# Optimization experiments

Hardware: AMD Instinct MI355X
Metric: run time of the kernel (lower is better)

The kernel has to match this reference:

```python
import jax, jax.numpy as jnp
import numpy as np

B = 64      # graphs per batch
N = 1024    # nodes per graph (equal-size graphs -> static top-k)
D = 256     # in_dim
DEG = 16    # avg degree
K = 512     # k = ratio * N, ratio = 0.5
E = B * N * DEG
NT = B * N


def setup_inputs() -> dict:
    key = jax.random.key(0)
    ks = jax.random.split(key, 8)
    feature = jax.random.normal(ks[0], (NT, D), jnp.float32)
    gid = jnp.repeat(jnp.arange(B), N * DEG)          # graph id per edge
    src = gid * N + jax.random.randint(ks[1], (E,), 0, N)
    dst = gid * N + jax.random.randint(ks[2], (E,), 0, N)
    label = jax.random.randint(ks[3], (B,), 0, 2)
    W = jax.random.normal(ks[4], (D, 1), jnp.float32) / np.sqrt(D)   # GraphConv weight
    b = jnp.zeros((1,), jnp.float32)                                  # GraphConv bias
    lin1_w = jax.random.normal(ks[5], (2, 1), jnp.float32) / np.sqrt(2.0)
    lin1_b = jnp.zeros((1,), jnp.float32)
    return dict(feature=feature, src=src, dst=dst, label=label,
                W=W, b=b, lin1_w=lin1_w, lin1_b=lin1_b)


def reference(feature, src, dst, label, W, b, lin1_w, lin1_b):
    fdt = feature.dtype
    # ---- get_bias_score: distance-to-class-center score ----
    node_label = jnp.repeat(label, N).astype(fdt)                 # [NT]
    gemb = feature.reshape(B, N, D).mean(axis=1)                  # AvgPooling per graph [B, D]
    lab_f = label.astype(fdt)                                     # [B]
    n1 = jnp.maximum(lab_f.sum(), 1.0)
    n0 = jnp.maximum((1.0 - lab_f).sum(), 1.0)
    center0 = (gemb * (1.0 - lab_f)[:, None]).sum(0) / n0         # [D]
    center1 = (gemb * lab_f[:, None]).sum(0) / n1                 # [D]
    d0 = jnp.sqrt(((feature - center0) ** 2).sum(-1))             # [NT]
    d1 = jnp.sqrt(((feature - center1) ** 2).sum(-1))             # [NT]
    score_distance = (d0 - d1) * ((node_label - 0.5) * 2.0)       # [NT]
    # ---- GraphConv(in_dim, 1), norm='both' (DGL semantics) ----
    ones_e = jnp.ones((E,), fdt)
    deg_out = jax.ops.segment_sum(ones_e, src, NT)
    deg_in = jax.ops.segment_sum(ones_e, dst, NT)
    ns = jnp.maximum(deg_out, 1.0) ** -0.5                        # src-side norm
    nd = jnp.maximum(deg_in, 1.0) ** -0.5                         # dst-side norm
    h = (feature @ W) * ns[:, None]                               # project first (out<in) [NT,1]
    agg = jax.ops.segment_sum(h[src], dst, NT)                    # [NT,1]
    score_gcn = (agg * nd[:, None] + b)[:, 0]                     # [NT]
    # ---- combine two scores with lin1: Linear(2, 1) ----
    score = jnp.stack([score_gcn, score_distance], axis=-1) @ lin1_w + lin1_b  # [NT,1]
    sflat = score[:, 0]
    # ---- per-graph top-k (mytopk with equal-size graphs -> static k) ----
    _, idx = jax.lax.top_k(sflat.reshape(B, N), K)                # [B,K] local indices
    perm = (idx + (jnp.arange(B) * N)[:, None]).reshape(-1)       # [B*K] global indices
    mask = jnp.ones((NT,), bool).at[perm].set(False)
    perm_com = jnp.nonzero(mask, size=NT - B * K)[0]              # complement, static size
    # ---- gather + tanh-gated features ----
    feature_dis = feature[perm] * jnp.tanh(sflat[perm])[:, None]          # [B*K, D]
    feature_com = feature[perm_com] * jnp.tanh(sflat[perm_com])[:, None]  # [B*(N-K), D]
    score_soft = jax.nn.softmax(score, axis=0)                    # softmax over all nodes
    return feature_dis, feature_com, perm, perm_com, score_soft
```

## Files before the change

kernel.cpp:

```cpp
#include <hip/hip_runtime.h>
#include <math.h>

#define Bg   64
#define Nn   1024
#define Dd   256
#define Ee   (Bg * Nn * 16)
#define EPG  16384
#define NT   (Bg * Nn)
#define Kk   512

#define OFF_DIS   0
#define OFF_COM   8388608
#define OFF_PERM  16777216
#define OFF_PCOM  16809984
#define OFF_SOFT  16842752

#define WS_SGCN    0
#define WS_H0      (NT * 4)
#define WS_SFLAT   (NT * 4 * 2)
#define WS_GPART   (NT * 4 * 3)
#define WS_C0      (WS_GPART + 512 * 256 * 4)
#define WS_C1      (WS_C0 + 1024)
#define WS_REDM    (WS_C1 + 1024)
#define WS_REDS    (WS_REDM + 256)
#define WS_PERMI   (WS_REDS + 256)
#define WS_PCOMI   (WS_PERMI + 32768 * 4)

__global__ void k_pass1(const float* __restrict__ f, const float* __restrict__ W,
                        float* __restrict__ gpart, float* __restrict__ h0) {
    __shared__ float scol[4 * Dd];
    int blk  = blockIdx.x;
    int base = blk * 128;
    int t    = threadIdx.x;
    int lane = t & 63, wid = t >> 6;
    const float4* f4 = (const float4*)f;
    const float4* W4 = (const float4*)W;
    float4 w = W4[lane];
    float4 cs = make_float4(0.f, 0.f, 0.f, 0.f);
    for (int r = 0; r < 32; ++r) {
        int row = base + wid * 32 + r;
        float4 v = f4[(size_t)row * 64 + lane];
        cs.x += v.x; cs.y += v.y; cs.z += v.z; cs.w += v.w;
        float d = v.x * w.x + v.y * w.y + v.z * w.z + v.w * w.w;
        for (int o = 32; o > 0; o >>= 1) d += __shfl_xor(d, o);
        if (lane == 0) h0[row] = d;
    }
    ((float4*)scol)[wid * 64 + lane] = cs;
    __syncthreads();
    float s = scol[t] + scol[Dd + t] + scol[2 * Dd + t] + scol[3 * Dd + t];
    gpart[blk * Dd + t] = s;
}

__global__ __launch_bounds__(1024) void k_edges(
        const int* __restrict__ src, const int* __restrict__ dst,
        const float* __restrict__ h0, const float* __restrict__ b,
        const float* __restrict__ gpart, const int* __restrict__ label,
        float* __restrict__ sgcn, float* __restrict__ c0, float* __restrict__ c1) {
    __shared__ ushort2 eb[EPG];
    __shared__ int   sdo[Nn];
    __shared__ int   sdi[Nn];
    __shared__ float sagg[Nn];
    __shared__ float shn[Nn];
    int g = blockIdx.x, t = threadIdx.x;
    sdo[t] = 0; sdi[t] = 0; sagg[t] = 0.f;
    __syncthreads();
    int ebase = g * EPG;
    const int4* s4 = (const int4*)(src + ebase);
    const int4* d4 = (const int4*)(dst + ebase);
    #pragma unroll
    for (int i = t; i < EPG / 4; i += 1024) {
        int4 ss = s4[i];
        int4 dd = d4[i];
        int s0 = ss.x & (Nn - 1), s1 = ss.y & (Nn - 1), s2 = ss.z & (Nn - 1), s3 = ss.w & (Nn - 1);
        int e0 = dd.x & (Nn - 1), e1 = dd.y & (Nn - 1), e2 = dd.z & (Nn - 1), e3 = dd.w & (Nn - 1);
        eb[i * 4 + 0] = make_ushort2((unsigned short)s0, (unsigned short)e0);
        eb[i * 4 + 1] = make_ushort2((unsigned short)s1, (unsigned short)e1);
        eb[i * 4 + 2] = make_ushort2((unsigned short)s2, (unsigned short)e2);
        eb[i * 4 + 3] = make_ushort2((unsigned short)s3, (unsigned short)e3);
        atomicAdd(&sdo[s0], 1); atomicAdd(&sdo[s1], 1);
        atomicAdd(&sdo[s2], 1); atomicAdd(&sdo[s3], 1);
        atomicAdd(&sdi[e0], 1); atomicAdd(&sdi[e1], 1);
        atomicAdd(&sdi[e2], 1); atomicAdd(&sdi[e3], 1);
    }
    __syncthreads();
    {
        int dg = sdo[t]; if (dg < 1) dg = 1;
        shn[t] = h0[g * Nn + t] / sqrtf((float)dg);
    }
    __syncthreads();
    #pragma unroll
    for (int i = t; i < EPG; i += 1024) {
        ushort2 e = eb[i];
        atomicAdd(&sagg[e.y], shn[e.x]);
    }
    __syncthreads();
    {
        int dg = sdi[t]; if (dg < 1) dg = 1;
        float nd = 1.f / sqrtf((float)dg);
        sgcn[g * Nn + t] = sagg[t] * nd + b[0];
    }
    if (g == 0 && t < Dd) {
        int n1 = 0;
        for (int gg = 0; gg < Bg; ++gg) n1 += label[gg];
        float fn1 = fmaxf((float)n1, 1.f);
        float fn0 = fmaxf((float)(Bg - n1), 1.f);
        float s0 = 0.f, s1 = 0.f;
        for (int gg = 0; gg < Bg; ++gg) {
            float v = 0.f;
            for (int p = 0; p < 8; ++p) v += gpart[(gg * 8 + p) * Dd + t];
            v *= (1.f / (float)Nn);
            if (label[gg]) s1 += v; else s0 += v;
        }
        c0[t] = s0 / fn0;
        c1[t] = s1 / fn1;
    }
}

__global__ void k_score(const float* __restrict__ f, const float* __restrict__ c0,
                        const float* __restrict__ c1, const float* __restrict__ sgcn,
                        const int* __restrict__ label, const float* __restrict__ lw,
                        const float* __restrict__ lb, float* __restrict__ sflat) {
    int node = blockIdx.x * 4 + (threadIdx.x >> 6);
    int lane = threadIdx.x & 63;
    const float4* f4  = (const float4*)f;
    const float4* c04 = (const float4*)c0;
    const float4* c14 = (const float4*)c1;
    float4 v = f4[(size_t)node * 64 + lane];
    float4 a = c04[lane];
    float4 bb = c14[lane];
    float dx, acc0, acc1;
    dx = v.x - a.x;  acc0  = dx * dx;
    dx = v.y - a.y;  acc0 += dx * dx;
    dx = v.z - a.z;  acc0 += dx * dx;
    dx = v.w - a.w;  acc0 += dx * dx;
    dx = v.x - bb.x; acc1  = dx * dx;
    dx = v.y - bb.y; acc1 += dx * dx;
    dx = v.z - bb.z; acc1 += dx * dx;
    dx = v.w - bb.w; acc1 += dx * dx;
    for (int o = 32; o > 0; o >>= 1) {
        acc0 += __shfl_xor(acc0, o);
        acc1 += __shfl_xor(acc1, o);
    }
    if (lane == 0) {
        float d0 = sqrtf(acc0), d1 = sqrtf(acc1);
        int g = node >> 10;
        float sgn = label[g] ? 1.f : -1.f;
        float sdist = (d0 - d1) * sgn;
        sflat[node] = sgcn[node] * lw[0] + sdist * lw[1] + lb[0];
    }
}

__global__ __launch_bounds__(512) void k_topk(
        const float* __restrict__ sflat, int* __restrict__ permI,
        int* __restrict__ pcomI, float* __restrict__ out,
        float* __restrict__ redM, float* __restrict__ redS) {
    __shared__ unsigned long long sk[1024];
    __shared__ int   sflag[1024];
    __shared__ int   swave[8];
    __shared__ float sred[16];
    int g = blockIdx.x, t = threadIdx.x;
    int lane = t & 63, w = t >> 6;
    float v0 = sflat[g * Nn + t];
    float v1 = sflat[g * Nn + t + 512];
    unsigned u0 = __float_as_uint(v0);
    unsigned u1 = __float_as_uint(v1);
    unsigned o0 = u0 ^ ((u0 >> 31) ? 0xFFFFFFFFu : 0x80000000u);
    unsigned o1 = u1 ^ ((u1 >> 31) ? 0xFFFFFFFFu : 0x80000000u);
    sk[t]       = ((unsigned long long)o0 << 32) | (unsigned)(1023 - t);
    sk[t + 512] = ((unsigned long long)o1 << 32) | (unsigned)(1023 - (t + 512));
    __syncthreads();
    for (int k = 2; k <= 1024; k <<= 1) {
        for (int j = k >> 1; j > 0; j >>= 1) {
            int l = ((t & ~(j - 1)) << 1) | (t & (j - 1));
            int r = l | j;
            unsigned long long a = sk[l], bk = sk[r];
            bool up = ((l & k) == 0);
            if ((a < bk) == up) { sk[l] = bk; sk[r] = a; }
            __syncthreads();
        }
    }
    sflag[t] = 1; sflag[t + 512] = 1;
    __syncthreads();
    {
        int loc = 1023 - (int)(sk[t] & 0xFFFFFFFFu);
        sflag[loc] = 0;
        int gi = g * Nn + loc;
        permI[g * Kk + t] = gi;
        out[OFF_PERM + g * Kk + t] = (float)gi;
    }
    __syncthreads();
    int f0 = sflag[2 * t], f1 = sflag[2 * t + 1];
    int f2 = f0 + f1;
    int inc = f2;
    for (int o = 1; o < 64; o <<= 1) {
        int y = __shfl_up(inc, o);
        if (lane >= o) inc += y;
    }
    if (lane == 63) swave[w] = inc;
    __syncthreads();
    if (t < 8) {
        int a = swave[t];
        for (int o = 1; o < 8; o <<= 1) {
            int y = __shfl_up(a, o);
            if (t >= o) a += y;
        }
        swave[t] = a;
    }
    __syncthreads();
    int basep = ((w > 0) ? swave[w - 1] : 0) + (inc - f2);
    if (f0) {
        int gi = g * Nn + 2 * t;
        pcomI[g * Kk + basep] = gi;
        out[OFF_PCOM + g * Kk + basep] = (float)gi;
    }
    if (f1) {
        int pos = basep + f0;
        int gi = g * Nn + 2 * t + 1;
        pcomI[g * Kk + pos] = gi;
        out[OFF_PCOM + g * Kk + pos] = (float)gi;
    }
    float m = fmaxf(v0, v1);
    for (int o = 32; o > 0; o >>= 1) m = fmaxf(m, __shfl_xor(m, o));
    if (lane == 0) sred[w] = m;
    __syncthreads();
    if (t < 8) {
        float a = sred[t];
        for (int o = 4; o > 0; o >>= 1) a = fmaxf(a, __shfl_xor(a, o));
        if (t == 0) sred[0] = a;
    }
    __syncthreads();
    m = sred[0];
    float s = expf(v0 - m) + expf(v1 - m);
    for (int o = 32; o > 0; o >>= 1) s += __shfl_xor(s, o);
    if (lane == 0) sred[8 + w] = s;
    __syncthreads();
    if (t < 8) {
        float a = sred[8 + t];
        for (int o = 4; o > 0; o >>= 1) a += __shfl_xor(a, o);
        if (t == 0) { redM[g] = m; redS[g] = a; }
    }
}

__global__ void k_write(const float* __restrict__ f, const int* __restrict__ permI,
                        const int* __restrict__ pcomI, const float* __restrict__ sflat,
                        const float* __restrict__ redM, const float* __restrict__ redS,
                        float* __restrict__ out) {
    __shared__ float sMS[2];
    int t = threadIdx.x;
    if (t < 64) {
        float m = redM[t];
        float mm = m;
        for (int o = 32; o > 0; o >>= 1) mm = fmaxf(mm, __shfl_xor(mm, o));
        float s = redS[t] * expf(m - mm);
        for (int o = 32; o > 0; o >>= 1) s += __shfl_xor(s, o);
        if (t == 0) { sMS[0] = mm; sMS[1] = s; }
    }
    __syncthreads();
    float M = sMS[0], S = sMS[1];
    if (t < 4) {
        int i = blockIdx.x * 4 + t;
        out[OFF_SOFT + i] = expf(sflat[i] - M) / S;
    }
    int j = blockIdx.x * 4 + (t >> 6);
    int lane = t & 63;
    int row = (j < 32768) ? permI[j] : pcomI[j - 32768];
    float tv = tanhf(sflat[row]);
    const float4* f4 = (const float4*)f;
    float4* o4 = (float4*)out;
    float4 v = f4[(size_t)row * 64 + lane];
    o4[(size_t)j * 64 + lane] = make_float4(v.x * tv, v.y * tv, v.z * tv, v.w * tv);
}

extern "C" void kernel_launch(void* const* d_in, const int* in_sizes, int n_in,
                              void* d_out, int out_size, void* d_ws, size_t ws_size,
                              hipStream_t stream) {
    const float* feature = (const float*)d_in[0];
    const int*   src     = (const int*)d_in[1];
    const int*   dst     = (const int*)d_in[2];
    const int*   label   = (const int*)d_in[3];
    const float* W       = (const float*)d_in[4];
    const float* b       = (const float*)d_in[5];
    const float* lw      = (const float*)d_in[6];
    const float* lb      = (const float*)d_in[7];
    float* out = (float*)d_out;
    char*  ws  = (char*)d_ws;

    float* sgcn    = (float*)(ws + WS_SGCN);
    float* h0      = (float*)(ws + WS_H0);
    float* sflat   = (float*)(ws + WS_SFLAT);
    float* gpart   = (float*)(ws + WS_GPART);
    float* c0      = (float*)(ws + WS_C0);
    float* c1      = (float*)(ws + WS_C1);
    float* redM    = (float*)(ws + WS_REDM);
    float* redS    = (float*)(ws + WS_REDS);
    int*   permI   = (int*)(ws + WS_PERMI);
    int*   pcomI   = (int*)(ws + WS_PCOMI);

    k_pass1<<<512, 256, 0, stream>>>(feature, W, gpart, h0);
    k_edges<<<Bg, 1024, 0, stream>>>(src, dst, h0, b, gpart, label, sgcn, c0, c1);
    k_score<<<NT / 4, 256, 0, stream>>>(feature, c0, c1, sgcn, label, lw, lb, sflat);
    k_topk<<<Bg, 512, 0, stream>>>(sflat, permI, pcomI, out, redM, redS);
    k_write<<<NT / 4, 256, 0, stream>>>(feature, permI, pcomI, sflat, redM, redS, out);
}
```

Before: 223.9 us.

## Split edge processing into 4 slices per graph and overlap with feature pass

```diff
diff --git a/kernel.cpp b/kernel.cpp
--- a/kernel.cpp
+++ b/kernel.cpp
@@ -6,6 +6,7 @@
 #define Dd   256
 #define Ee   (Bg * Nn * 16)
 #define EPG  16384
+#define EPB  4096
 #define NT   (Bg * Nn)
 #define Kk   512
 
@@ -15,91 +16,115 @@
 #define OFF_PCOM  16809984
 #define OFF_SOFT  16842752
 
-#define WS_SGCN    0
-#define WS_H0      (NT * 4)
-#define WS_SFLAT   (NT * 4 * 2)
-#define WS_GPART   (NT * 4 * 3)
+#define WS_H0      0
+#define WS_SFLAT   (NT * 4)
+#define WS_GPART   (NT * 4 * 2)
 #define WS_C0      (WS_GPART + 512 * 256 * 4)
 #define WS_C1      (WS_C0 + 1024)
 #define WS_REDM    (WS_C1 + 1024)
 #define WS_REDS    (WS_REDM + 256)
 #define WS_PERMI   (WS_REDS + 256)
 #define WS_PCOMI   (WS_PERMI + 32768 * 4)
-
-__global__ void k_pass1(const float* __restrict__ f, const float* __restrict__ W,
-                        float* __restrict__ gpart, float* __restrict__ h0) {
-    __shared__ float scol[4 * Dd];
-    int blk  = blockIdx.x;
-    int base = blk * 128;
-    int t    = threadIdx.x;
-    int lane = t & 63, wid = t >> 6;
-    const float4* f4 = (const float4*)f;
-    const float4* W4 = (const float4*)W;
-    float4 w = W4[lane];
-    float4 cs = make_float4(0.f, 0.f, 0.f, 0.f);
-    for (int r = 0; r < 32; ++r) {
-        int row = base + wid * 32 + r;
-        float4 v = f4[(size_t)row * 64 + lane];
-        cs.x += v.x; cs.y += v.y; cs.z += v.z; cs.w += v.w;
-        float d = v.x * w.x + v.y * w.y + v.z * w.z + v.w * w.w;
-        for (int o = 32; o > 0; o >>= 1) d += __shfl_xor(d, o);
-        if (lane == 0) h0[row] = d;
-    }
-    ((float4*)scol)[wid * 64 + lane] = cs;
-    __syncthreads();
-    float s = scol[t] + scol[Dd + t] + scol[2 * Dd + t] + scol[3 * Dd + t];
-    gpart[blk * Dd + t] = s;
-}
-
-__global__ __launch_bounds__(1024) void k_edges(
+#define WS_EPACK   (WS_PCOMI + 32768 * 4)
+#define WS_DO4     (WS_EPACK + Ee * 4)
+#define WS_DI4     (WS_DO4 + 4 * NT * 4)
+#define WS_AGG4    (WS_DI4 + 4 * NT * 4)
+
+__global__ __launch_bounds__(256) void k_mix(
+        const float* __restrict__ f, const float* __restrict__ W,
         const int* __restrict__ src, const int* __restrict__ dst,
-        const float* __restrict__ h0, const float* __restrict__ b,
-        const float* __restrict__ gpart, const int* __restrict__ label,
-        float* __restrict__ sgcn, float* __restrict__ c0, float* __restrict__ c1) {
-    __shared__ ushort2 eb[EPG];
-    __shared__ int   sdo[Nn];
-    __shared__ int   sdi[Nn];
+        float* __restrict__ gpart, float* __restrict__ h0,
+        unsigned* __restrict__ epack, int* __restrict__ do4, int* __restrict__ di4) {
+    __shared__ int smem[2048];
+    int blk = blockIdx.x;
+    int t   = threadIdx.x;
+    if (blk < 512) {
+        float* scol = (float*)smem;
+        int base = blk * 128;
+        int lane = t & 63, wid = t >> 6;
+        const float4* f4 = (const float4*)f;
+        const float4* W4 = (const float4*)W;
+        float4 w = W4[lane];
+        float4 cs = make_float4(0.f, 0.f, 0.f, 0.f);
+        for (int r = 0; r < 32; ++r) {
+            int row = base + wid * 32 + r;
+            float4 v = f4[(size_t)row * 64 + lane];
+            cs.x += v.x; cs.y += v.y; cs.z += v.z; cs.w += v.w;
+            float d = v.x * w.x + v.y * w.y + v.z * w.z + v.w * w.w;
+            for (int o = 32; o > 0; o >>= 1) d += __shfl_xor(d, o);
+            if (lane == 0) h0[row] = d;
+        }
+        ((float4*)scol)[wid * 64 + lane] = cs;
+        __syncthreads();
+        float s = scol[t] + scol[Dd + t] + scol[2 * Dd + t] + scol[3 * Dd + t];
+        gpart[blk * Dd + t] = s;
+    } else {
+        int* sdo = smem;
+        int* sdi = smem + 1024;
+        int blk2 = blk - 512;
+        int g = blk2 >> 2, sl = blk2 & 3;
+        #pragma unroll
+        for (int j = 0; j < 4; ++j) { sdo[t + j * 256] = 0; sdi[t + j * 256] = 0; }
+        __syncthreads();
+        int ebase = g * EPG + sl * EPB;
+        const int4* s4 = (const int4*)(src + ebase);
+        const int4* d4 = (const int4*)(dst + ebase);
+        uint4* p4 = (uint4*)(epack + ebase);
+        #pragma unroll
+        for (int i = t; i < EPB / 4; i += 256) {
+            int4 ss = s4[i];
+            int4 dd = d4[i];
+            int s0 = ss.x & (Nn - 1), s1 = ss.y & (Nn - 1), s2 = ss.z & (Nn - 1), s3 = ss.w & (Nn - 1);
+            int e0 = dd.x & (Nn - 1), e1 = dd.y & (Nn - 1), e2 = dd.z & (Nn - 1), e3 = dd.w & (Nn - 1);
+            uint4 pk;
+            pk.x = (unsigned)(s0 | (e0 << 16));
+            pk.y = (unsigned)(s1 | (e1 << 16));
+            pk.z = (unsigned)(s2 | (e2 << 16));
+            pk.w = (unsigned)(s3 | (e3 << 16));
+            p4[i] = pk;
+            atomicAdd(&sdo[s0], 1); atomicAdd(&sdo[s1], 1);
+            atomicAdd(&sdo[s2], 1); atomicAdd(&sdo[s3], 1);
+            atomicAdd(&sdi[e0], 1); atomicAdd(&sdi[e1], 1);
+            atomicAdd(&sdi[e2], 1); atomicAdd(&sdi[e3], 1);
+        }
+        __syncthreads();
+        int base = sl * NT + g * Nn;
+        #pragma unroll
+        for (int j = 0; j < 4; ++j) {
+            do4[base + t + j * 256] = sdo[t + j * 256];
+            di4[base + t + j * 256] = sdi[t + j * 256];
+        }
+    }
+}
+
+__global__ __launch_bounds__(1024) void k_edgeB(
+        const unsigned* __restrict__ epack, const float* __restrict__ h0,
+        const int* __restrict__ do4, const float* __restrict__ gpart,
+        const int* __restrict__ label, float* __restrict__ agg4,
+        float* __restrict__ c0, float* __restrict__ c1) {
+    __shared__ float shn[Nn];
     __shared__ float sagg[Nn];
-    __shared__ float shn[Nn];
-    int g = blockIdx.x, t = threadIdx.x;
-    sdo[t] = 0; sdi[t] = 0; sagg[t] = 0.f;
-    __syncthreads();
-    int ebase = g * EPG;
-    const int4* s4 = (const int4*)(src + ebase);
-    const int4* d4 = (const int4*)(dst + ebase);
-    #pragma unroll
-    for (int i = t; i < EPG / 4; i += 1024) {
-        int4 ss = s4[i];
-        int4 dd = d4[i];
-        int s0 = ss.x & (Nn - 1), s1 = ss.y & (Nn - 1), s2 = ss.z & (Nn - 1), s3 = ss.w & (Nn - 1);
-        int e0 = dd.x & (Nn - 1), e1 = dd.y & (Nn - 1), e2 = dd.z & (Nn - 1), e3 = dd.w & (Nn - 1);
-        eb[i * 4 + 0] = make_ushort2((unsigned short)s0, (unsigned short)e0);
-        eb[i * 4 + 1] = make_ushort2((unsigned short)s1, (unsigned short)e1);
-        eb[i * 4 + 2] = make_ushort2((unsigned short)s2, (unsigned short)e2);
-        eb[i * 4 + 3] = make_ushort2((unsigned short)s3, (unsigned short)e3);
-        atomicAdd(&sdo[s0], 1); atomicAdd(&sdo[s1], 1);
-        atomicAdd(&sdo[s2], 1); atomicAdd(&sdo[s3], 1);
-        atomicAdd(&sdi[e0], 1); atomicAdd(&sdi[e1], 1);
-        atomicAdd(&sdi[e2], 1); atomicAdd(&sdi[e3], 1);
-    }
-    __syncthreads();
+    int blk = blockIdx.x, t = threadIdx.x;
+    int g = blk >> 2, sl = blk & 3;
     {
-        int dg = sdo[t]; if (dg < 1) dg = 1;
-        shn[t] = h0[g * Nn + t] / sqrtf((float)dg);
-    }
-    __syncthreads();
-    #pragma unroll
-    for (int i = t; i < EPG; i += 1024) {
-        ushort2 e = eb[i];
-        atomicAdd(&sagg[e.y], shn[e.x]);
+        int idx = g * Nn + t;
+        int dg = do4[idx] + do4[NT + idx] + do4[2 * NT + idx] + do4[3 * NT + idx];
+        if (dg < 1) dg = 1;
+        shn[t] = h0[idx] / sqrtf((float)dg);
+        sagg[t] = 0.f;
     }
     __syncthreads();
     {
-        int dg = sdi[t]; if (dg < 1) dg = 1;
-        float nd = 1.f / sqrtf((float)dg);
-        sgcn[g * Nn + t] = sagg[t] * nd + b[0];
-    }
-    if (g == 0 && t < Dd) {
+        const uint4* p4 = (const uint4*)(epack + g * EPG + sl * EPB);
+        uint4 pk = p4[t];
+        atomicAdd(&sagg[pk.x >> 16], shn[pk.x & 0xFFFF]);
+        atomicAdd(&sagg[pk.y >> 16], shn[pk.y & 0xFFFF]);
+        atomicAdd(&sagg[pk.z >> 16], shn[pk.z & 0xFFFF]);
+        atomicAdd(&sagg[pk.w >> 16], shn[pk.w & 0xFFFF]);
+    }
+    __syncthreads();
+    agg4[sl * NT + g * Nn + t] = sagg[t];
+    if (blk == 0 && t < Dd) {
         int n1 = 0;
         for (int gg = 0; gg < Bg; ++gg) n1 += label[gg];
         float fn1 = fmaxf((float)n1, 1.f);
@@ -117,8 +142,9 @@
 }
 
 __global__ void k_score(const float* __restrict__ f, const float* __restrict__ c0,
-                        const float* __restrict__ c1, const float* __restrict__ sgcn,
-                        const int* __restrict__ label, const float* __restrict__ lw,
+                        const float* __restrict__ c1, const float* __restrict__ agg4,
+                        const int* __restrict__ di4, const int* __restrict__ label,
+                        const float* __restrict__ b, const float* __restrict__ lw,
                         const float* __restrict__ lb, float* __restrict__ sflat) {
     int node = blockIdx.x * 4 + (threadIdx.x >> 6);
     int lane = threadIdx.x & 63;
@@ -146,7 +172,11 @@
         int g = node >> 10;
         float sgn = label[g] ? 1.f : -1.f;
         float sdist = (d0 - d1) * sgn;
-        sflat[node] = sgcn[node] * lw[0] + sdist * lw[1] + lb[0];
+        float agg = agg4[node] + agg4[NT + node] + agg4[2 * NT + node] + agg4[3 * NT + node];
+        int dg = di4[node] + di4[NT + node] + di4[2 * NT + node] + di4[3 * NT + node];
+        if (dg < 1) dg = 1;
+        float sgcn = agg / sqrtf((float)dg) + b[0];
+        sflat[node] = sgcn * lw[0] + sdist * lw[1] + lb[0];
     }
 }
 
@@ -285,20 +315,23 @@
     float* out = (float*)d_out;
     char*  ws  = (char*)d_ws;
 
-    float* sgcn    = (float*)(ws + WS_SGCN);
-    float* h0      = (float*)(ws + WS_H0);
-    float* sflat   = (float*)(ws + WS_SFLAT);
-    float* gpart   = (float*)(ws + WS_GPART);
-    float* c0      = (float*)(ws + WS_C0);
-    float* c1      = (float*)(ws + WS_C1);
-    float* redM    = (float*)(ws + WS_REDM);
-    float* redS    = (float*)(ws + WS_REDS);
-    int*   permI   = (int*)(ws + WS_PERMI);
-    int*   pcomI   = (int*)(ws + WS_PCOMI);
-
-    k_pass1<<<512, 256, 0, stream>>>(feature, W, gpart, h0);
-    k_edges<<<Bg, 1024, 0, stream>>>(src, dst, h0, b, gpart, label, sgcn, c0, c1);
-    k_score<<<NT / 4, 256, 0, stream>>>(feature, c0, c1, sgcn, label, lw, lb, sflat);
+    float*    h0    = (float*)(ws + WS_H0);
+    float*    sflat = (float*)(ws + WS_SFLAT);
+    float*    gpart = (float*)(ws + WS_GPART);
+    float*    c0    = (float*)(ws + WS_C0);
+    float*    c1    = (float*)(ws + WS_C1);
+    float*    redM  = (float*)(ws + WS_REDM);
+    float*    redS  = (float*)(ws + WS_REDS);
+    int*      permI = (int*)(ws + WS_PERMI);
+    int*      pcomI = (int*)(ws + WS_PCOMI);
+    unsigned* epack = (unsigned*)(ws + WS_EPACK);
+    int*      do4   = (int*)(ws + WS_DO4);
+    int*      di4   = (int*)(ws + WS_DI4);
+    float*    agg4  = (float*)(ws + WS_AGG4);
+
+    k_mix<<<768, 256, 0, stream>>>(feature, W, src, dst, gpart, h0, epack, do4, di4);
+    k_edgeB<<<256, 1024, 0, stream>>>(epack, h0, do4, gpart, label, agg4, c0, c1);
+    k_score<<<NT / 4, 256, 0, stream>>>(feature, c0, c1, agg4, di4, label, b, lw, lb, sflat);
     k_topk<<<Bg, 512, 0, stream>>>(sflat, permI, pcomI, out, redM, redS);
     k_write<<<NT / 4, 256, 0, stream>>>(feature, permI, pcomI, sflat, redM, redS, out);
 }
```

After: 211.0 us. 1.06x faster.

## Fuse all stages into one persistent kernel with software grid barriers

Applied to the files above, without the earlier changes.

```diff
diff --git a/kernel.cpp b/kernel.cpp
--- a/kernel.cpp
+++ b/kernel.cpp
@@ -4,271 +4,300 @@
 #define Bg   64
 #define Nn   1024
 #define Dd   256
-#define Ee   (Bg * Nn * 16)
 #define EPG  16384
-#define NT   (Bg * Nn)
+#define EPB  4096
+#define NT   65536
 #define Kk   512
 
-#define OFF_DIS   0
-#define OFF_COM   8388608
 #define OFF_PERM  16777216
 #define OFF_PCOM  16809984
 #define OFF_SOFT  16842752
 
-#define WS_SGCN    0
-#define WS_H0      (NT * 4)
-#define WS_SFLAT   (NT * 4 * 2)
-#define WS_GPART   (NT * 4 * 3)
-#define WS_C0      (WS_GPART + 512 * 256 * 4)
-#define WS_C1      (WS_C0 + 1024)
-#define WS_REDM    (WS_C1 + 1024)
-#define WS_REDS    (WS_REDM + 256)
-#define WS_PERMI   (WS_REDS + 256)
-#define WS_PCOMI   (WS_PERMI + 32768 * 4)
-
-__global__ void k_pass1(const float* __restrict__ f, const float* __restrict__ W,
-                        float* __restrict__ gpart, float* __restrict__ h0) {
-    __shared__ float scol[4 * Dd];
-    int blk  = blockIdx.x;
-    int base = blk * 128;
-    int t    = threadIdx.x;
-    int lane = t & 63, wid = t >> 6;
-    const float4* f4 = (const float4*)f;
-    const float4* W4 = (const float4*)W;
-    float4 w = W4[lane];
-    float4 cs = make_float4(0.f, 0.f, 0.f, 0.f);
-    for (int r = 0; r < 32; ++r) {
-        int row = base + wid * 32 + r;
-        float4 v = f4[(size_t)row * 64 + lane];
-        cs.x += v.x; cs.y += v.y; cs.z += v.z; cs.w += v.w;
-        float d = v.x * w.x + v.y * w.y + v.z * w.z + v.w * w.w;
-        for (int o = 32; o > 0; o >>= 1) d += __shfl_xor(d, o);
-        if (lane == 0) h0[row] = d;
-    }
-    ((float4*)scol)[wid * 64 + lane] = cs;
-    __syncthreads();
-    float s = scol[t] + scol[Dd + t] + scol[2 * Dd + t] + scol[3 * Dd + t];
-    gpart[blk * Dd + t] = s;
+#define WS_BAR    0
+#define WS_H0     256
+#define WS_SFLAT  (WS_H0 + NT * 4)
+#define WS_GPART  (WS_SFLAT + NT * 4)
+#define WS_DO4    (WS_GPART + 256 * 256 * 4)
+#define WS_DI4    (WS_DO4 + 4 * NT * 4)
+#define WS_AGG4   (WS_DI4 + 4 * NT * 4)
+#define WS_REDM   (WS_AGG4 + 4 * NT * 4)
+#define WS_REDS   (WS_REDM + 256 * 4)
+#define WS_PERMI  (WS_REDS + 256 * 4)
+#define WS_PCOMI  (WS_PERMI + 32768 * 4)
+
+__device__ __forceinline__ void gridbar(int* ctr, int target) {
+    __syncthreads();
+    if (threadIdx.x == 0) {
+        __threadfence();
+        __hip_atomic_fetch_add(ctr, 1, __ATOMIC_RELEASE, __HIP_MEMORY_SCOPE_AGENT);
+        while (__hip_atomic_load(ctr, __ATOMIC_ACQUIRE, __HIP_MEMORY_SCOPE_AGENT) < target)
+            __builtin_amdgcn_s_sleep(8);
+        __threadfence();
+    }
+    __syncthreads();
 }
 
-__global__ __launch_bounds__(1024) void k_edges(
+__global__ __launch_bounds__(1024, 4) void k_all(
+        const float* __restrict__ f, const float* __restrict__ W,
         const int* __restrict__ src, const int* __restrict__ dst,
-        const float* __restrict__ h0, const float* __restrict__ b,
-        const float* __restrict__ gpart, const int* __restrict__ label,
-        float* __restrict__ sgcn, float* __restrict__ c0, float* __restrict__ c1) {
-    __shared__ ushort2 eb[EPG];
+        const int* __restrict__ label, const float* __restrict__ bias,
+        const float* __restrict__ lw, const float* __restrict__ lb,
+        float* __restrict__ out, int* __restrict__ bar,
+        float* __restrict__ h0, float* __restrict__ sflat,
+        float* __restrict__ gpart, int* __restrict__ do4, int* __restrict__ di4,
+        float* __restrict__ agg4, float* __restrict__ redM, float* __restrict__ redS,
+        int* __restrict__ permI, int* __restrict__ pcomI) {
+    __shared__ unsigned epk[EPB];
+    __shared__ float scol[4096];
     __shared__ int   sdo[Nn];
     __shared__ int   sdi[Nn];
+    __shared__ float shn[Nn];
     __shared__ float sagg[Nn];
-    __shared__ float shn[Nn];
-    int g = blockIdx.x, t = threadIdx.x;
-    sdo[t] = 0; sdi[t] = 0; sagg[t] = 0.f;
-    __syncthreads();
-    int ebase = g * EPG;
-    const int4* s4 = (const int4*)(src + ebase);
-    const int4* d4 = (const int4*)(dst + ebase);
-    #pragma unroll
-    for (int i = t; i < EPG / 4; i += 1024) {
-        int4 ss = s4[i];
-        int4 dd = d4[i];
-        int s0 = ss.x & (Nn - 1), s1 = ss.y & (Nn - 1), s2 = ss.z & (Nn - 1), s3 = ss.w & (Nn - 1);
-        int e0 = dd.x & (Nn - 1), e1 = dd.y & (Nn - 1), e2 = dd.z & (Nn - 1), e3 = dd.w & (Nn - 1);
-        eb[i * 4 + 0] = make_ushort2((unsigned short)s0, (unsigned short)e0);
-        eb[i * 4 + 1] = make_ushort2((unsigned short)s1, (unsigned short)e1);
-        eb[i * 4 + 2] = make_ushort2((unsigned short)s2, (unsigned short)e2);
-        eb[i * 4 + 3] = make_ushort2((unsigned short)s3, (unsigned short)e3);
+    __shared__ float cpart[2048];
+    __shared__ float c0s[Dd], c1s[Dd];
+    __shared__ unsigned long long sk[1024];
+    __shared__ int   sflag[1024];
+    __shared__ int   swave[8];
+    __shared__ float sred[16];
+
+    int b = blockIdx.x, t = threadIdx.x;
+    int lane = t & 63, w = t >> 6;
+    int g = b >> 2, sl = b & 3;
+    const float4* f4 = (const float4*)f;
+
+    sdo[t] = 0; sdi[t] = 0;
+    int4 ss = ((const int4*)(src + g * EPG + sl * EPB))[t];
+    int4 dd = ((const int4*)(dst + g * EPG + sl * EPB))[t];
+    __syncthreads();
+    {
+        float4 wv = ((const float4*)W)[lane];
+        float4 cs = make_float4(0.f, 0.f, 0.f, 0.f);
+        int rbase = b * 256 + w * 16;
+        for (int r = 0; r < 16; ++r) {
+            float4 v = f4[(size_t)(rbase + r) * 64 + lane];
+            cs.x += v.x; cs.y += v.y; cs.z += v.z; cs.w += v.w;
+            float d = v.x * wv.x + v.y * wv.y + v.z * wv.z + v.w * wv.w;
+            for (int o = 32; o > 0; o >>= 1) d += __shfl_xor(d, o);
+            if (lane == 0) h0[rbase + r] = d;
+        }
+        ((float4*)scol)[w * 64 + lane] = cs;
+    }
+    {
+        int s0 = ss.x & 1023, s1 = ss.y & 1023, s2 = ss.z & 1023, s3 = ss.w & 1023;
+        int e0 = dd.x & 1023, e1 = dd.y & 1023, e2 = dd.z & 1023, e3 = dd.w & 1023;
+        uint4 pk;
+        pk.x = (unsigned)(s0 | (e0 << 16));
+        pk.y = (unsigned)(s1 | (e1 << 16));
+        pk.z = (unsigned)(s2 | (e2 << 16));
+        pk.w = (unsigned)(s3 | (e3 << 16));
+        ((uint4*)epk)[t] = pk;
         atomicAdd(&sdo[s0], 1); atomicAdd(&sdo[s1], 1);
         atomicAdd(&sdo[s2], 1); atomicAdd(&sdo[s3], 1);
         atomicAdd(&sdi[e0], 1); atomicAdd(&sdi[e1], 1);
         atomicAdd(&sdi[e2], 1); atomicAdd(&sdi[e3], 1);
     }
     __syncthreads();
-    {
-        int dg = sdo[t]; if (dg < 1) dg = 1;
-        shn[t] = h0[g * Nn + t] / sqrtf((float)dg);
-    }
-    __syncthreads();
-    #pragma unroll
-    for (int i = t; i < EPG; i += 1024) {
-        ushort2 e = eb[i];
-        atomicAdd(&sagg[e.y], shn[e.x]);
-    }
-    __syncthreads();
-    {
-        int dg = sdi[t]; if (dg < 1) dg = 1;
-        float nd = 1.f / sqrtf((float)dg);
-        sgcn[g * Nn + t] = sagg[t] * nd + b[0];
-    }
-    if (g == 0 && t < Dd) {
+    if (t < 256) {
+        float s = 0.f;
+        for (int q = 0; q < 16; ++q) s += scol[q * 256 + t];
+        gpart[b * 256 + t] = s;
+    }
+    do4[sl * NT + g * Nn + t] = sdo[t];
+    di4[sl * NT + g * Nn + t] = sdi[t];
+    gridbar(bar, 256);
+
+    {
+        int q = t >> 8, c = t & 255;
         int n1 = 0;
         for (int gg = 0; gg < Bg; ++gg) n1 += label[gg];
-        float fn1 = fmaxf((float)n1, 1.f);
-        float fn0 = fmaxf((float)(Bg - n1), 1.f);
         float s0 = 0.f, s1 = 0.f;
-        for (int gg = 0; gg < Bg; ++gg) {
-            float v = 0.f;
-            for (int p = 0; p < 8; ++p) v += gpart[(gg * 8 + p) * Dd + t];
-            v *= (1.f / (float)Nn);
-            if (label[gg]) s1 += v; else s0 += v;
-        }
-        c0[t] = s0 / fn0;
-        c1[t] = s1 / fn1;
-    }
-}
-
-__global__ void k_score(const float* __restrict__ f, const float* __restrict__ c0,
-                        const float* __restrict__ c1, const float* __restrict__ sgcn,
-                        const int* __restrict__ label, const float* __restrict__ lw,
-                        const float* __restrict__ lb, float* __restrict__ sflat) {
-    int node = blockIdx.x * 4 + (threadIdx.x >> 6);
-    int lane = threadIdx.x & 63;
-    const float4* f4  = (const float4*)f;
-    const float4* c04 = (const float4*)c0;
-    const float4* c14 = (const float4*)c1;
-    float4 v = f4[(size_t)node * 64 + lane];
-    float4 a = c04[lane];
-    float4 bb = c14[lane];
-    float dx, acc0, acc1;
-    dx = v.x - a.x;  acc0  = dx * dx;
-    dx = v.y - a.y;  acc0 += dx * dx;
-    dx = v.z - a.z;  acc0 += dx * dx;
-    dx = v.w - a.w;  acc0 += dx * dx;
-    dx = v.x - bb.x; acc1  = dx * dx;
-    dx = v.y - bb.y; acc1 += dx * dx;
-    dx = v.z - bb.z; acc1 += dx * dx;
-    dx = v.w - bb.w; acc1 += dx * dx;
-    for (int o = 32; o > 0; o >>= 1) {
-        acc0 += __shfl_xor(acc0, o);
-        acc1 += __shfl_xor(acc1, o);
-    }
-    if (lane == 0) {
-        float d0 = sqrtf(acc0), d1 = sqrtf(acc1);
-        int g = node >> 10;
+        for (int bb2 = q * 64; bb2 < q * 64 + 64; ++bb2) {
+            float v = gpart[bb2 * 256 + c];
+            if (label[bb2 >> 2]) s1 += v; else s0 += v;
+        }
+        cpart[q * 256 + c] = s0;
+        cpart[1024 + q * 256 + c] = s1;
+        __syncthreads();
+        if (t < 256) {
+            float a0 = cpart[t] + cpart[256 + t] + cpart[512 + t] + cpart[768 + t];
+            float a1 = cpart[1024 + t] + cpart[1280 + t] + cpart[1536 + t] + cpart[1792 + t];
+            float fn1 = fmaxf((float)n1, 1.f);
+            float fn0 = fmaxf((float)(Bg - n1), 1.f);
+            c0s[t] = (a0 / (float)Nn) / fn0;
+            c1s[t] = (a1 / (float)Nn) / fn1;
+        }
+    }
+    {
+        int node = g * Nn + t;
+        int dg = do4[node] + do4[NT + node] + do4[2 * NT + node] + do4[3 * NT + node];
+        if (dg < 1) dg = 1;
+        shn[t] = h0[node] / sqrtf((float)dg);
+        sagg[t] = 0.f;
+    }
+    __syncthreads();
+    {
+        uint4 pk = ((const uint4*)epk)[t];
+        atomicAdd(&sagg[pk.x >> 16], shn[pk.x & 0xFFFF]);
+        atomicAdd(&sagg[pk.y >> 16], shn[pk.y & 0xFFFF]);
+        atomicAdd(&sagg[pk.z >> 16], shn[pk.z & 0xFFFF]);
+        atomicAdd(&sagg[pk.w >> 16], shn[pk.w & 0xFFFF]);
+    }
+    __syncthreads();
+    agg4[sl * NT + g * Nn + t] = sagg[t];
+    gridbar(bar, 512);
+
+    {
+        float4 a = ((const float4*)c0s)[lane];
+        float4 bb4 = ((const float4*)c1s)[lane];
         float sgn = label[g] ? 1.f : -1.f;
-        float sdist = (d0 - d1) * sgn;
-        sflat[node] = sgcn[node] * lw[0] + sdist * lw[1] + lb[0];
-    }
-}
-
-__global__ __launch_bounds__(512) void k_topk(
-        const float* __restrict__ sflat, int* __restrict__ permI,
-        int* __restrict__ pcomI, float* __restrict__ out,
-        float* __restrict__ redM, float* __restrict__ redS) {
-    __shared__ unsigned long long sk[1024];
-    __shared__ int   sflag[1024];
-    __shared__ int   swave[8];
-    __shared__ float sred[16];
-    int g = blockIdx.x, t = threadIdx.x;
-    int lane = t & 63, w = t >> 6;
-    float v0 = sflat[g * Nn + t];
-    float v1 = sflat[g * Nn + t + 512];
-    unsigned u0 = __float_as_uint(v0);
-    unsigned u1 = __float_as_uint(v1);
-    unsigned o0 = u0 ^ ((u0 >> 31) ? 0xFFFFFFFFu : 0x80000000u);
-    unsigned o1 = u1 ^ ((u1 >> 31) ? 0xFFFFFFFFu : 0x80000000u);
-    sk[t]       = ((unsigned long long)o0 << 32) | (unsigned)(1023 - t);
-    sk[t + 512] = ((unsigned long long)o1 << 32) | (unsigned)(1023 - (t + 512));
-    __syncthreads();
-    for (int k = 2; k <= 1024; k <<= 1) {
-        for (int j = k >> 1; j > 0; j >>= 1) {
-            int l = ((t & ~(j - 1)) << 1) | (t & (j - 1));
-            int r = l | j;
-            unsigned long long a = sk[l], bk = sk[r];
-            bool up = ((l & k) == 0);
-            if ((a < bk) == up) { sk[l] = bk; sk[r] = a; }
-            __syncthreads();
-        }
-    }
-    sflag[t] = 1; sflag[t + 512] = 1;
-    __syncthreads();
-    {
-        int loc = 1023 - (int)(sk[t] & 0xFFFFFFFFu);
-        sflag[loc] = 0;
-        int gi = g * Nn + loc;
-        permI[g * Kk + t] = gi;
-        out[OFF_PERM + g * Kk + t] = (float)gi;
-    }
-    __syncthreads();
-    int f0 = sflag[2 * t], f1 = sflag[2 * t + 1];
-    int f2 = f0 + f1;
-    int inc = f2;
-    for (int o = 1; o < 64; o <<= 1) {
-        int y = __shfl_up(inc, o);
-        if (lane >= o) inc += y;
-    }
-    if (lane == 63) swave[w] = inc;
-    __syncthreads();
-    if (t < 8) {
-        int a = swave[t];
-        for (int o = 1; o < 8; o <<= 1) {
-            int y = __shfl_up(a, o);
-            if (t >= o) a += y;
-        }
-        swave[t] = a;
-    }
-    __syncthreads();
-    int basep = ((w > 0) ? swave[w - 1] : 0) + (inc - f2);
-    if (f0) {
-        int gi = g * Nn + 2 * t;
-        pcomI[g * Kk + basep] = gi;
-        out[OFF_PCOM + g * Kk + basep] = (float)gi;
-    }
-    if (f1) {
-        int pos = basep + f0;
-        int gi = g * Nn + 2 * t + 1;
-        pcomI[g * Kk + pos] = gi;
-        out[OFF_PCOM + g * Kk + pos] = (float)gi;
-    }
-    float m = fmaxf(v0, v1);
-    for (int o = 32; o > 0; o >>= 1) m = fmaxf(m, __shfl_xor(m, o));
-    if (lane == 0) sred[w] = m;
-    __syncthreads();
-    if (t < 8) {
-        float a = sred[t];
-        for (int o = 4; o > 0; o >>= 1) a = fmaxf(a, __shfl_xor(a, o));
-        if (t == 0) sred[0] = a;
-    }
-    __syncthreads();
-    m = sred[0];
-    float s = expf(v0 - m) + expf(v1 - m);
-    for (int o = 32; o > 0; o >>= 1) s += __shfl_xor(s, o);
-    if (lane == 0) sred[8 + w] = s;
-    __syncthreads();
-    if (t < 8) {
-        float a = sred[8 + t];
-        for (int o = 4; o > 0; o >>= 1) a += __shfl_xor(a, o);
-        if (t == 0) { redM[g] = m; redS[g] = a; }
-    }
-}
-
-__global__ void k_write(const float* __restrict__ f, const int* __restrict__ permI,
-                        const int* __restrict__ pcomI, const float* __restrict__ sflat,
-                        const float* __restrict__ redM, const float* __restrict__ redS,
-                        float* __restrict__ out) {
-    __shared__ float sMS[2];
-    int t = threadIdx.x;
-    if (t < 64) {
-        float m = redM[t];
-        float mm = m;
-        for (int o = 32; o > 0; o >>= 1) mm = fmaxf(mm, __shfl_xor(mm, o));
-        float s = redS[t] * expf(m - mm);
-        for (int o = 32; o > 0; o >>= 1) s += __shfl_xor(s, o);
-        if (t == 0) { sMS[0] = mm; sMS[1] = s; }
-    }
-    __syncthreads();
-    float M = sMS[0], S = sMS[1];
-    if (t < 4) {
-        int i = blockIdx.x * 4 + t;
-        out[OFF_SOFT + i] = expf(sflat[i] - M) / S;
-    }
-    int j = blockIdx.x * 4 + (t >> 6);
-    int lane = t & 63;
-    int row = (j < 32768) ? permI[j] : pcomI[j - 32768];
-    float tv = tanhf(sflat[row]);
-    const float4* f4 = (const float4*)f;
-    float4* o4 = (float4*)out;
-    float4 v = f4[(size_t)row * 64 + lane];
-    o4[(size_t)j * 64 + lane] = make_float4(v.x * tv, v.y * tv, v.z * tv, v.w * tv);
+        float blw0 = lw[0], blw1 = lw[1], blb = lb[0], bbias = bias[0];
+        int rbase = b * 256 + w * 16;
+        for (int r = 0; r < 16; ++r) {
+            int node = rbase + r;
+            float4 v = f4[(size_t)node * 64 + lane];
+            float dx, acc0, acc1;
+            dx = v.x - a.x;   acc0  = dx * dx;
+            dx = v.y - a.y;   acc0 += dx * dx;
+            dx = v.z - a.z;   acc0 += dx * dx;
+            dx = v.w - a.w;   acc0 += dx * dx;
+            dx = v.x - bb4.x; acc1  = dx * dx;
+            dx = v.y - bb4.y; acc1 += dx * dx;
+            dx = v.z - bb4.z; acc1 += dx * dx;
+            dx = v.w - bb4.w; acc1 += dx * dx;
+            for (int o = 32; o > 0; o >>= 1) {
+                acc0 += __shfl_xor(acc0, o);
+                acc1 += __shfl_xor(acc1, o);
+            }
+            if (lane == 0) {
+                float sdist = (sqrtf(acc0) - sqrtf(acc1)) * sgn;
+                float agg = agg4[node] + agg4[NT + node] + agg4[2 * NT + node] + agg4[3 * NT + node];
+                int dg = di4[node] + di4[NT + node] + di4[2 * NT + node] + di4[3 * NT + node];
+                if (dg < 1) dg = 1;
+                float sg = agg / sqrtf((float)dg) + bbias;
+                float sc = sg * blw0 + sdist * blw1 + blb;
+                sflat[node] = sc;
+                scol[w * 16 + r] = sc;
+            }
+        }
+        __syncthreads();
+        if (t < 256) {
+            float m = scol[t];
+            for (int o = 32; o > 0; o >>= 1) m = fmaxf(m, __shfl_xor(m, o));
+            if (lane == 0) sred[t >> 6] = m;
+        }
+        __syncthreads();
+        if (t == 0) sred[8] = fmaxf(fmaxf(sred[0], sred[1]), fmaxf(sred[2], sred[3]));
+        __syncthreads();
+        float M = sred[8];
+        if (t < 256) {
+            float e = expf(scol[t] - M);
+            for (int o = 32; o > 0; o >>= 1) e += __shfl_xor(e, o);
+            if (lane == 0) sred[4 + (t >> 6)] = e;
+        }
+        __syncthreads();
+        if (t == 0) { redM[b] = M; redS[b] = sred[4] + sred[5] + sred[6] + sred[7]; }
+    }
+    gridbar(bar, 768);
+
+    if (b < Bg) {
+        int gg = b;
+        float v = sflat[gg * Nn + t];
+        unsigned u = __float_as_uint(v);
+        unsigned od = u ^ ((u >> 31) ? 0xFFFFFFFFu : 0x80000000u);
+        sk[t] = ((unsigned long long)od << 32) | (unsigned)(1023 - t);
+        __syncthreads();
+        for (int k = 2; k <= 1024; k <<= 1) {
+            for (int j = k >> 1; j > 0; j >>= 1) {
+                if (t < 512) {
+                    int l = ((t & ~(j - 1)) << 1) | (t & (j - 1));
+                    int r = l | j;
+                    unsigned long long a = sk[l], bk = sk[r];
+                    bool up = ((l & k) == 0);
+                    if ((a < bk) == up) { sk[l] = bk; sk[r] = a; }
+                }
+                __syncthreads();
+            }
+        }
+        sflag[t] = 1;
+        __syncthreads();
+        if (t < 512) {
+            int loc = 1023 - (int)(sk[t] & 0xFFFFFFFFu);
+            sflag[loc] = 0;
+            int gi = gg * Nn + loc;
+            permI[gg * Kk + t] = gi;
+            out[OFF_PERM + gg * Kk + t] = (float)gi;
+        }
+        __syncthreads();
+        int f0 = 0, f1 = 0, inc = 0, fsum = 0;
+        if (t < 512) {
+            f0 = sflag[2 * t]; f1 = sflag[2 * t + 1];
+            fsum = f0 + f1;
+            inc = fsum;
+            for (int o = 1; o < 64; o <<= 1) {
+                int y = __shfl_up(inc, o);
+                if (lane >= o) inc += y;
+            }
+            if (lane == 63) swave[w] = inc;
+        }
+        __syncthreads();
+        if (t < 8) {
+            int a = swave[t];
+            for (int o = 1; o < 8; o <<= 1) {
+                int y = __shfl_up(a, o);
+                if (t >= o) a += y;
+            }
+            swave[t] = a;
+        }
+        __syncthreads();
+        if (t < 512) {
+            int basep = ((w > 0) ? swave[w - 1] : 0) + (inc - fsum);
+            if (f0) {
+                int gi = gg * Nn + 2 * t;
+                pcomI[gg * Kk + basep] = gi;
+                out[OFF_PCOM + gg * Kk + basep] = (float)gi;
+            }
+            if (f1) {
+                int pos = basep + f0;
+                int gi = gg * Nn + 2 * t + 1;
+                pcomI[gg * Kk + pos] = gi;
+                out[OFF_PCOM + gg * Kk + pos] = (float)gi;
+            }
+        }
+    }
+    gridbar(bar, 1024);
+
+    {
+        if (t < 256) {
+            float m = redM[t];
+            for (int o = 32; o > 0; o >>= 1) m = fmaxf(m, __shfl_xor(m, o));
+            if (lane == 0) sred[t >> 6] = m;
+        }
+        __syncthreads();
+        if (t == 0) sred[8] = fmaxf(fmaxf(sred[0], sred[1]), fmaxf(sred[2], sred[3]));
+        __syncthreads();
+        float M = sred[8];
+        if (t < 256) {
+            float s = redS[t] * expf(redM[t] - M);
+            for (int o = 32; o > 0; o >>= 1) s += __shfl_xor(s, o);
+            if (lane == 0) sred[4 + (t >> 6)] = s;
+        }
+        __syncthreads();
+        if (t == 0) sred[9] = sred[4] + sred[5] + sred[6] + sred[7];
+        __syncthreads();
+        float S = sred[9];
+        if (t < 256) {
+            int node = b * 256 + t;
+            out[OFF_SOFT + node] = expf(sflat[node] - M) / S;
+        }
+        for (int r = 0; r < 16; ++r) {
+            int j = b * 256 + w * 16 + r;
+            int row = (j < 32768) ? permI[j] : pcomI[j - 32768];
+            float tv = tanhf(sflat[row]);
+            float4 v = f4[(size_t)row * 64 + lane];
+            ((float4*)out)[(size_t)j * 64 + lane] =
+                make_float4(v.x * tv, v.y * tv, v.z * tv, v.w * tv);
+        }
+    }
 }
 
 extern "C" void kernel_launch(void* const* d_in, const int* in_sizes, int n_in,
@@ -279,26 +308,26 @@
     const int*   dst     = (const int*)d_in[2];
     const int*   label   = (const int*)d_in[3];
     const float* W       = (const float*)d_in[4];
-    const float* b       = (const float*)d_in[5];
+    const float* bias    = (const float*)d_in[5];
     const float* lw      = (const float*)d_in[6];
     const float* lb      = (const float*)d_in[7];
     float* out = (float*)d_out;
     char*  ws  = (char*)d_ws;
 
-    float* sgcn    = (float*)(ws + WS_SGCN);
-    float* h0      = (float*)(ws + WS_H0);
-    float* sflat   = (float*)(ws + WS_SFLAT);
-    float* gpart   = (float*)(ws + WS_GPART);
-    float* c0      = (float*)(ws + WS_C0);
-    float* c1      = (float*)(ws + WS_C1);
-    float* redM    = (float*)(ws + WS_REDM);
-    float* redS    = (float*)(ws + WS_REDS);
-    int*   permI   = (int*)(ws + WS_PERMI);
-    int*   pcomI   = (int*)(ws + WS_PCOMI);
-
-    k_pass1<<<512, 256, 0, stream>>>(feature, W, gpart, h0);
-    k_edges<<<Bg, 1024, 0, stream>>>(src, dst, h0, b, gpart, label, sgcn, c0, c1);
-    k_score<<<NT / 4, 256, 0, stream>>>(feature, c0, c1, sgcn, label, lw, lb, sflat);
-    k_topk<<<Bg, 512, 0, stream>>>(sflat, permI, pcomI, out, redM, redS);
-    k_write<<<NT / 4, 256, 0, stream>>>(feature, permI, pcomI, sflat, redM, redS, out);
+    int*   bar   = (int*)(ws + WS_BAR);
+    float* h0    = (float*)(ws + WS_H0);
+    float* sflat = (float*)(ws + WS_SFLAT);
+    float* gpart = (float*)(ws + WS_GPART);
+    int*   do4   = (int*)(ws + WS_DO4);
+    int*   di4   = (int*)(ws + WS_DI4);
+    float* agg4  = (float*)(ws + WS_AGG4);
+    float* redM  = (float*)(ws + WS_REDM);
+    float* redS  = (float*)(ws + WS_REDS);
+    int*   permI = (int*)(ws + WS_PERMI);
+    int*   pcomI = (int*)(ws + WS_PCOMI);
+
+    hipMemsetAsync(ws + WS_BAR, 0, 64, stream);
+    k_all<<<256, 1024, 0, stream>>>(feature, W, src, dst, label, bias, lw, lb,
+                                    out, bar, h0, sflat, gpart, do4, di4, agg4,
+                                    redM, redS, permI, pcomI);
 }
```

New measurement: 300.0 us. 1.34x slower.
